# Optimization experiments

Measured on AMD Instinct MI355X. Metric: run time of the kernel, lower is better.

The kernel has to match this reference:

```python
import jax, jax.numpy as jnp
import numpy as np

N_NODES = 100000
N_EDGES = 600000
EMB_DIM = 128
NUM_LAYER = 3
NUM_GRAPHS = 64


def setup_inputs() -> dict:
    key = jax.random.key(0)
    ks = jax.random.split(key, 10)
    s = 1.0 / np.sqrt(EMB_DIM)  # keep activations stable through stacked GEMMs
    return {
        "x": jax.random.randint(ks[0], (N_NODES, 2), 0, 2),
        "edge_index_pos": jax.random.randint(ks[1], (2, N_EDGES), 0, N_NODES),
        "edge_index_inv": jax.random.randint(ks[2], (2, N_EDGES), 0, N_NODES),
        "batch": jnp.sort(jax.random.randint(ks[3], (N_NODES,), 0, NUM_GRAPHS)),
        "type_emb": jax.random.normal(ks[4], (14, EMB_DIM), jnp.float32),
        "output_emb": jax.random.normal(ks[5], (2, EMB_DIM), jnp.float32),
        "lin1_w": jax.random.normal(ks[6], (NUM_LAYER, 2, EMB_DIM, EMB_DIM), jnp.float32) * s,
        "lin1_b": jnp.zeros((NUM_LAYER, 2, EMB_DIM), jnp.float32),
        "lin2_w": jax.random.normal(ks[7], (NUM_LAYER, 2, EMB_DIM, EMB_DIM), jnp.float32) * s,
        "lin2_b": jnp.zeros((NUM_LAYER, 2, EMB_DIM), jnp.float32),
    }


def _gin_rel(h, ei, w1, b1, w2, b2):
    # GINConv (eps=0): MLP(x + sum_{j in N(i)} x_j); messages flow src(row0)->dst(row1)
    agg = jax.ops.segment_sum(h[ei[0]], ei[1], num_segments=h.shape[0])
    z = jax.nn.relu((h + agg) @ w1 + b1)
    return z @ w2 + b2


def reference(x, edge_index_pos, edge_index_inv, batch, type_emb, output_emb,
              lin1_w, lin1_b, lin2_w, lin2_b):
    # node input embedding: type + output-flag
    h = type_emb[x[:, 0]] + output_emb[x[:, 1]]
    num_layer = lin1_w.shape[0]
    for l in range(num_layer):  # small fixed layer loop
        hn = (_gin_rel(h, edge_index_pos, lin1_w[l, 0], lin1_b[l, 0], lin2_w[l, 0], lin2_b[l, 0])
              + _gin_rel(h, edge_index_inv, lin1_w[l, 1], lin1_b[l, 1], lin2_w[l, 1], lin2_b[l, 1]))
        h = hn if l == num_layer - 1 else jax.nn.relu(hn)  # JK='last', drop_ratio=0
    node_rep = h
    # MultiAggregation(['sum','mean','max','min']) pooling by graph id
    sum_g = jax.ops.segment_sum(node_rep, batch, num_segments=NUM_GRAPHS)
    cnt = jax.ops.segment_sum(jnp.ones((node_rep.shape[0],), node_rep.dtype), batch, num_segments=NUM_GRAPHS)
    mean_g = sum_g / jnp.maximum(cnt, 1.0)[:, None]
    max_g = jax.ops.segment_max(node_rep, batch, num_segments=NUM_GRAPHS)
    min_g = jax.ops.segment_min(node_rep, batch, num_segments=NUM_GRAPHS)
    h_graph = jnp.concatenate([sum_g, mean_g, max_g, min_g], axis=1)  # [B, 4*D]
    h_graph = h_graph.reshape(NUM_GRAPHS, -1, 4).transpose(0, 2, 1)   # [B, 4, D] (interleaved as in torch view)
    batch_mask = jnp.ones((NUM_GRAPHS, 4), dtype=bool)
    return (h_graph, batch_mask)
```

## Files before the change

kernel.cpp:

```cpp
#include <hip/hip_runtime.h>
#include <stdint.h>

#define M_NODES 100000
#define M_PAD   100096
#define NE      600000
#define DIM     128
#define NGRAPH  64
#define SCAN_B  512
#define SCAN_NB ((M_NODES + SCAN_B - 1) / SCAN_B)
#define WP      136

typedef __attribute__((ext_vector_type(8))) short short8;
typedef __attribute__((ext_vector_type(4))) float f32x4;
typedef __attribute__((ext_vector_type(4))) unsigned int u32x4;

__device__ inline float bf2lo(uint32_t u) { return __uint_as_float(u << 16); }
__device__ inline float bf2hi(uint32_t u) { return __uint_as_float(u & 0xffff0000u); }
__device__ inline uint32_t packbf2(float a, float b) {
    uint32_t ua = __float_as_uint(a), ub = __float_as_uint(b);
    ua += 0x7fffu + ((ua >> 16) & 1u);
    ub += 0x7fffu + ((ub >> 16) & 1u);
    return (ua >> 16) | (ub & 0xffff0000u);
}
__device__ inline uint16_t ftobf16(float f) {
    uint32_t u = __float_as_uint(f);
    u += 0x7fffu + ((u >> 16) & 1u);
    return (uint16_t)(u >> 16);
}

__device__ inline void async_copy16(const uint16_t* g, uint16_t* l) {
    __builtin_amdgcn_global_load_lds(
        (const __attribute__((address_space(1))) uint32_t*)g,
        (__attribute__((address_space(3))) uint32_t*)l, 16, 0, 0);
}

__device__ inline u32x4 gload16(const u32x4* p) {
    u32x4 r;
    asm volatile("global_load_dwordx4 %0, %1, off" : "=&v"(r) : "v"(p));
    return r;
}

#define GB_EMBED 25000
#define GB_TRANS (GB_EMBED + 12)
#define GB_ZERO  (GB_TRANS + 391)
#define GB_BOUND (GB_ZERO + 391)
__global__ void k_setup(const int* __restrict__ x, const float2* __restrict__ te2,
                        const float2* __restrict__ oe2, uint32_t* __restrict__ h2,
                        const float* __restrict__ w1, const float* __restrict__ w2,
                        uint16_t* __restrict__ wfrag,
                        const int* __restrict__ batch, int* __restrict__ starts,
                        int* __restrict__ degp, int* __restrict__ degi) {
    int b = blockIdx.x, t = threadIdx.x;
    if (b < GB_EMBED) {
        int id = b * 256 + t;
        int node = id >> 6, p = id & 63;
        int x0 = x[node * 2], x1 = x[node * 2 + 1];
        float2 a = te2[x0 * 64 + p], bb = oe2[x1 * 64 + p];
        h2[node * 64 + p] = packbf2(a.x + bb.x, a.y + bb.y);
    } else if (b < GB_TRANS) {
        int m = b - GB_EMBED;
        const float* src;
        uint16_t* dst;
        if (m < 6) {
            int L = m >> 1, rel = m & 1;
            src = w1 + m * 16384;
            dst = wfrag + (size_t)(L * 4 + rel) * 16384;
        } else {
            int mm = m - 6, L = mm >> 1, rel = mm & 1;
            src = w2 + mm * 16384;
            dst = wfrag + (size_t)(L * 4 + 2 + rel) * 16384;
        }
        for (int o = t; o < 16384; o += 256) {
            int f = o >> 3, j = o & 7;
            int fb = f >> 6, ln = f & 63;
            int t_ = fb >> 2, s_ = fb & 3, qq = ln >> 4, ll = ln & 15;
            dst[o] = ftobf16(src[(s_ * 32 + qq * 8 + j) * 128 + t_ * 16 + ll]);
        }
    } else if (b < GB_ZERO) {
        int i = (b - GB_TRANS) * 256 + t;
        if (i < M_NODES) { degp[i] = 0; degi[i] = 0; }
    } else {
        int i = (b - GB_ZERO) * 256 + t;
        if (i >= M_NODES) return;
        int bb = batch[i];
        int pb = (i == 0) ? -1 : batch[i - 1];
        for (int g = pb + 1; g <= bb; ++g) starts[g] = i;
        if (i == M_NODES - 1)
            for (int g = bb + 1; g <= NGRAPH; ++g) starts[g] = M_NODES;
    }
}

__global__ void k_hist(const int* __restrict__ ep, const int* __restrict__ ei,
                       int* __restrict__ degp, int* __restrict__ degi,
                       int* __restrict__ slotp, int* __restrict__ sloti) {
    int e = blockIdx.x * blockDim.x + threadIdx.x;
    if (e >= NE) return;
    slotp[e] = atomicAdd(&degp[ep[NE + e]], 1);
    sloti[e] = atomicAdd(&degi[ei[NE + e]], 1);
}

__global__ void k_scan1(const int* __restrict__ degp, const int* __restrict__ degi,
                        int* __restrict__ rsp, int* __restrict__ rsi, int* __restrict__ bsum) {
    __shared__ int s[SCAN_B];
    int list = blockIdx.y;
    const int* deg = list ? degi : degp;
    int* rs = list ? rsi : rsp;
    int i = blockIdx.x * SCAN_B + threadIdx.x;
    int v = (i < M_NODES) ? deg[i] : 0;
    s[threadIdx.x] = v;
    __syncthreads();
    for (int off = 1; off < SCAN_B; off <<= 1) {
        int xv = (threadIdx.x >= off) ? s[threadIdx.x - off] : 0;
        __syncthreads();
        s[threadIdx.x] += xv;
        __syncthreads();
    }
    if (i < M_NODES) rs[i + 1] = s[threadIdx.x];
    if (threadIdx.x == SCAN_B - 1) bsum[list * SCAN_NB + blockIdx.x] = s[threadIdx.x];
}

__global__ void k_scan2(const int* __restrict__ bsum, int* __restrict__ boff) {
    __shared__ int s[256];
    int list = blockIdx.x, t = threadIdx.x;
    int v = (t < SCAN_NB) ? bsum[list * SCAN_NB + t] : 0;
    s[t] = v;
    __syncthreads();
    for (int off = 1; off < 256; off <<= 1) {
        int xv = (t >= off) ? s[t - off] : 0;
        __syncthreads();
        s[t] += xv;
        __syncthreads();
    }
    if (t < SCAN_NB) boff[list * SCAN_NB + t] = s[t] - v;
}

__global__ void k_scan3(int* __restrict__ rsp, int* __restrict__ rsi, const int* __restrict__ boff) {
    int list = blockIdx.y;
    int* rs = list ? rsi : rsp;
    int i = blockIdx.x * SCAN_B + threadIdx.x;
    if (i < M_NODES) rs[i + 1] += boff[list * SCAN_NB + blockIdx.x];
    if (i == 0 && list == 0) { rsp[0] = 0; rsi[0] = 0; }
}

__global__ void k_fill(const int* __restrict__ ep, const int* __restrict__ ei,
                       const int* __restrict__ rsp, const int* __restrict__ rsi,
                       const int* __restrict__ slotp, const int* __restrict__ sloti,
                       int* __restrict__ csrp, int* __restrict__ csri) {
    int e = blockIdx.x * blockDim.x + threadIdx.x;
    if (e >= NE) return;
    int dp = ep[NE + e], sp = ep[e], kp = slotp[e];
    int di = ei[NE + e], si = ei[e], ki = sloti[e];
    csrp[rsp[dp] + kp] = sp;
    csri[rsi[di] + ki] = si;
}

__device__ inline void add8v(float* a, u32x4 v) {
    a[0] += bf2lo(v[0]); a[1] += bf2hi(v[0]);
    a[2] += bf2lo(v[1]); a[3] += bf2hi(v[1]);
    a[4] += bf2lo(v[2]); a[5] += bf2hi(v[2]);
    a[6] += bf2lo(v[3]); a[7] += bf2hi(v[3]);
}

#define AGG_W 3
__global__ void k_aggregate2(const u32x4* __restrict__ h4,
                             const int* __restrict__ rsp, const int* __restrict__ csrp,
                             const int* __restrict__ rsi, const int* __restrict__ csri,
                             u32x4* __restrict__ up, u32x4* __restrict__ ui) {
    int id = blockIdx.x * blockDim.x + threadIdx.x;
    int node = id >> 4, p = id & 15;
    if (node >= M_NODES) return;
    u32x4 hv = h4[(size_t)node * 16 + p];
    float a[8] = {bf2lo(hv[0]), bf2hi(hv[0]), bf2lo(hv[1]), bf2hi(hv[1]),
                  bf2lo(hv[2]), bf2hi(hv[2]), bf2lo(hv[3]), bf2hi(hv[3])};
    float b[8];
#pragma unroll
    for (int j = 0; j < 8; ++j) b[j] = a[j];
    int ea = rsp[node], e1a = rsp[node + 1];
    int eb = rsi[node], e1b = rsi[node + 1];
    int la = max(e1a - 1, 0);
    int lb = max(e1b - 1, 0);
    int da = e1a - ea, db = e1b - eb;
    int work = max(da, db);
    for (int done = 0; done < work; done += AGG_W) {
        int i0 = csrp[min(ea + done + 0, la)];
        int i1 = csrp[min(ea + done + 1, la)];
        int i2 = csrp[min(ea + done + 2, la)];
        int j0 = csri[min(eb + done + 0, lb)];
        int j1 = csri[min(eb + done + 1, lb)];
        int j2 = csri[min(eb + done + 2, lb)];
        u32x4 va0 = gload16(h4 + ((size_t)i0 * 16 + p));
        u32x4 va1 = gload16(h4 + ((size_t)i1 * 16 + p));
        u32x4 va2 = gload16(h4 + ((size_t)i2 * 16 + p));
        u32x4 vb0 = gload16(h4 + ((size_t)j0 * 16 + p));
        u32x4 vb1 = gload16(h4 + ((size_t)j1 * 16 + p));
        u32x4 vb2 = gload16(h4 + ((size_t)j2 * 16 + p));
        asm volatile("s_waitcnt vmcnt(0)"
                     : "+v"(va0), "+v"(va1), "+v"(va2),
                       "+v"(vb0), "+v"(vb1), "+v"(vb2));
        const u32x4 z4 = {0u, 0u, 0u, 0u};
        add8v(a, (done + 0 < da) ? va0 : z4);
        add8v(a, (done + 1 < da) ? va1 : z4);
        add8v(a, (done + 2 < da) ? va2 : z4);
        add8v(b, (done + 0 < db) ? vb0 : z4);
        add8v(b, (done + 1 < db) ? vb1 : z4);
        add8v(b, (done + 2 < db) ? vb2 : z4);
    }
    u32x4 oa, ob;
    oa[0] = packbf2(a[0], a[1]); oa[1] = packbf2(a[2], a[3]);
    oa[2] = packbf2(a[4], a[5]); oa[3] = packbf2(a[6], a[7]);
    ob[0] = packbf2(b[0], b[1]); ob[1] = packbf2(b[2], b[3]);
    ob[2] = packbf2(b[4], b[5]); ob[3] = packbf2(b[6], b[7]);
    up[(size_t)node * 16 + p] = oa;
    ui[(size_t)node * 16 + p] = ob;
}

__launch_bounds__(256, 2)
__global__ void k_gemm2(const uint16_t* __restrict__ Up, const uint16_t* __restrict__ Ui,
                        const uint16_t* __restrict__ WF1p, const float* __restrict__ B1p,
                        const uint16_t* __restrict__ WF2p, const float* __restrict__ B2p,
                        const uint16_t* __restrict__ WF1i, const float* __restrict__ B1i,
                        const uint16_t* __restrict__ WF2i, const float* __restrict__ B2i,
                        float* __restrict__ HN, uint16_t* __restrict__ HOUT, int last) {
    __shared__ __align__(16) uint16_t wbuf[16384];
    __shared__ __align__(16) uint16_t sZ[2][64 * WP];
    int tid = threadIdx.x;
    int wave = tid >> 6, lane = tid & 63;
    int q = lane >> 4, l16 = lane & 15;
    int rb0 = blockIdx.x * 128 + wave * 16;
    int rb1 = rb0 + 64;

    auto loadA = [&](const uint16_t* U, int rowbase, short8* v) {
        const uint16_t* P = U + (size_t)(rowbase + l16) * DIM + q * 8;
#pragma unroll
        for (int s = 0; s < 4; ++s) v[s] = *(const short8*)(P + s * 32);
    };
    auto loadw = [&](const uint16_t* WF) {
#pragma unroll
        for (int k = 0; k < 8; ++k)
            async_copy16(WF + (size_t)(tid + k * 256) * 8,
                         &wbuf[(size_t)wave * 512 + (size_t)k * 2048]);
    };
    auto stage1 = [&](const short8* af, const float* B1, int zslot) {
        f32x4 acc1[8];
#pragma unroll
        for (int t = 0; t < 8; ++t) acc1[t] = (f32x4){0.f, 0.f, 0.f, 0.f};
#pragma unroll
        for (int t = 0; t < 8; ++t)
#pragma unroll
            for (int s = 0; s < 4; ++s) {
                short8 bb = *(const short8*)&wbuf[((t * 4 + s) * 64 + lane) * 8];
                acc1[t] = __builtin_amdgcn_mfma_f32_16x16x32_bf16(af[s], bb, acc1[t], 0, 0, 0);
            }
#pragma unroll
        for (int t = 0; t < 8; ++t) {
            float b1v = B1[t * 16 + l16];
#pragma unroll
            for (int r = 0; r < 4; ++r)
                sZ[zslot][(wave * 16 + q * 4 + r) * WP + t * 16 + l16] =
                    ftobf16(fmaxf(acc1[t][r] + b1v, 0.f));
        }
    };
    auto stage2 = [&](int zslot, f32x4* acc2) {
        short8 zf[4];
#pragma unroll
        for (int s = 0; s < 4; ++s)
            zf[s] = *(const short8*)&sZ[zslot][(wave * 16 + l16) * WP + s * 32 + q * 8];
#pragma unroll
        for (int t = 0; t < 8; ++t)
#pragma unroll
            for (int s = 0; s < 4; ++s) {
                short8 bb = *(const short8*)&wbuf[((t * 4 + s) * 64 + lane) * 8];
                acc2[t] = __builtin_amdgcn_mfma_f32_16x16x32_bf16(zf[s], bb, acc2[t], 0, 0, 0);
            }
    };

    f32x4 acc2a[8], acc2b[8];
#pragma unroll
    for (int t = 0; t < 8; ++t) { acc2a[t] = (f32x4){0.f,0.f,0.f,0.f}; acc2b[t] = (f32x4){0.f,0.f,0.f,0.f}; }

    short8 af0[4], af1[4];
    loadw(WF1p);
    loadA(Up, rb0, af0); loadA(Up, rb1, af1);
    __syncthreads();
    stage1(af0, B1p, 0); stage1(af1, B1p, 1);
    __syncthreads();
    loadw(WF2p); __syncthreads();
    stage2(0, acc2a); stage2(1, acc2b);
    __syncthreads();
    loadw(WF1i);
    loadA(Ui, rb0, af0); loadA(Ui, rb1, af1);
    __syncthreads();
    stage1(af0, B1i, 0); stage1(af1, B1i, 1);
    __syncthreads();
    loadw(WF2i); __syncthreads();
    stage2(0, acc2a); stage2(1, acc2b);

#pragma unroll
    for (int t = 0; t < 8; ++t) {
        int col = t * 16 + l16;
        float b2v = B2p[col] + B2i[col];
#pragma unroll
        for (int r = 0; r < 4; ++r) {
            int row0 = rb0 + q * 4 + r, row1 = rb1 + q * 4 + r;
            float y0 = acc2a[t][r] + b2v, y1 = acc2b[t][r] + b2v;
            if (last) {
                HN[(size_t)row0 * DIM + col] = y0;
                HN[(size_t)row1 * DIM + col] = y1;
            } else {
                HOUT[(size_t)row0 * DIM + col] = ftobf16(fmaxf(y0, 0.f));
                HOUT[(size_t)row1 * DIM + col] = ftobf16(fmaxf(y1, 0.f));
            }
        }
    }
}

__global__ void k_pool1(const float* __restrict__ HN, const int* __restrict__ starts,
                        float* __restrict__ psum, float* __restrict__ pmax, float* __restrict__ pmin) {
    int g = blockIdx.x, sp = blockIdx.y, t = threadIdx.x;
    int d = t & 127, rh = t >> 7;
    int slot = sp * 2 + rh;
    int s0 = starts[g], s1 = starts[g + 1];
    float s = 0.f, mx = -INFINITY, mn = INFINITY;
    for (int i = s0 + slot; i < s1; i += 32) {
        float v = HN[(size_t)i * DIM + d];
        s += v; mx = fmaxf(mx, v); mn = fminf(mn, v);
    }
    int o = (g * 32 + slot) * DIM + d;
    psum[o] = s; pmax[o] = mx; pmin[o] = mn;
}

__global__ void k_pool2(const float* __restrict__ psum, const float* __restrict__ pmax,
                        const float* __restrict__ pmin, const int* __restrict__ starts,
                        float* __restrict__ out) {
    __shared__ float S[4][128];
    int g = blockIdx.x, t = threadIdx.x;
    float s = 0.f, mx = -INFINITY, mn = INFINITY;
    for (int p = 0; p < 32; ++p) {
        int o = (g * 32 + p) * DIM + t;
        s += psum[o]; mx = fmaxf(mx, pmax[o]); mn = fminf(mn, pmin[o]);
    }
    float cnt = (float)(starts[g + 1] - starts[g]);
    float mean = s / fmaxf(cnt, 1.f);
    S[0][t] = s; S[1][t] = mean; S[2][t] = mx; S[3][t] = mn;
    __syncthreads();
#pragma unroll
    for (int k = 0; k < 4; ++k) {
        int j = 4 * t + k;
        out[g * 512 + k * 128 + t] = S[j >> 7][j & 127];
    }
    if (t < 4) out[NGRAPH * 512 + g * 4 + t] = 1.0f;
}

extern "C" void kernel_launch(void* const* d_in, const int* in_sizes, int n_in,
                              void* d_out, int out_size, void* d_ws, size_t ws_size,
                              hipStream_t stream) {
    const int* x     = (const int*)d_in[0];
    const int* ep    = (const int*)d_in[1];
    const int* ei    = (const int*)d_in[2];
    const int* batch = (const int*)d_in[3];
    const float* te  = (const float*)d_in[4];
    const float* oe  = (const float*)d_in[5];
    const float* w1  = (const float*)d_in[6];
    const float* b1  = (const float*)d_in[7];
    const float* w2  = (const float*)d_in[8];
    const float* b2  = (const float*)d_in[9];
    float* out = (float*)d_out;

    char* w = (char*)d_ws;
    auto alloc = [&](size_t n) { char* p = w; w += (n + 255) & ~(size_t)255; return p; };
    uint16_t* h_bf  = (uint16_t*)alloc((size_t)M_PAD * DIM * 2);
    uint16_t* u_pos = (uint16_t*)alloc((size_t)M_PAD * DIM * 2);
    uint16_t* u_inv = (uint16_t*)alloc((size_t)M_PAD * DIM * 2);
    float*    hn    = (float*)alloc((size_t)M_PAD * DIM * 4);
    uint16_t* wfrag = (uint16_t*)alloc((size_t)12 * 16384 * 2);
    int* rsp  = (int*)alloc((M_NODES + 2) * 4);
    int* rsi  = (int*)alloc((M_NODES + 2) * 4);
    int* degp = (int*)alloc(M_NODES * 4);
    int* degi = (int*)alloc(M_NODES * 4);
    int* csrp = (int*)alloc((size_t)NE * 4);
    int* csri = (int*)alloc((size_t)NE * 4);
    int* bsum = (int*)alloc(2 * SCAN_NB * 4);
    int* boff = (int*)alloc(2 * SCAN_NB * 4);
    int* starts = (int*)alloc((NGRAPH + 1) * 4);
    float* psum = (float*)alloc(NGRAPH * 32 * DIM * 4);
    float* pmax = (float*)alloc(NGRAPH * 32 * DIM * 4);
    float* pmin = (float*)alloc(NGRAPH * 32 * DIM * 4);
    if ((size_t)(w - (char*)d_ws) > ws_size) return;

    int* slotp = (int*)u_pos;
    int* sloti = (int*)u_inv;

    k_setup<<<GB_BOUND, 256, 0, stream>>>(x, (const float2*)te, (const float2*)oe,
                                          (uint32_t*)h_bf, w1, w2, wfrag,
                                          batch, starts, degp, degi);
    k_hist<<<(NE + 255) / 256, 256, 0, stream>>>(ep, ei, degp, degi, slotp, sloti);
    dim3 gs(SCAN_NB, 2);
    k_scan1<<<gs, SCAN_B, 0, stream>>>(degp, degi, rsp, rsi, bsum);
    k_scan2<<<2, 256, 0, stream>>>(bsum, boff);
    k_scan3<<<gs, SCAN_B, 0, stream>>>(rsp, rsi, boff);
    k_fill<<<(NE + 255) / 256, 256, 0, stream>>>(ep, ei, rsp, rsi, slotp, sloti, csrp, csri);

    for (int l = 0; l < 3; ++l) {
        k_aggregate2<<<(M_NODES * 16 + 255) / 256, 256, 0, stream>>>(
            (const u32x4*)h_bf, rsp, csrp, rsi, csri, (u32x4*)u_pos, (u32x4*)u_inv);
        const uint16_t* wfL = wfrag + (size_t)l * 4 * 16384;
        k_gemm2<<<M_PAD / 128, 256, 0, stream>>>(
            u_pos, u_inv,
            wfL,              b1 + (2 * l) * 128,
            wfL + 2 * 16384,  b2 + (2 * l) * 128,
            wfL + 16384,      b1 + (2 * l + 1) * 128,
            wfL + 3 * 16384,  b2 + (2 * l + 1) * 128,
            hn, h_bf, (l == 2) ? 1 : 0);
    }
    dim3 gp(NGRAPH, 16);
    k_pool1<<<gp, 256, 0, stream>>>(hn, starts, psum, pmax, pmin);
    k_pool2<<<NGRAPH, 128, 0, stream>>>(psum, pmax, pmin, starts, out);
}
```

Baseline: 456.5 us.

## Bucket-sort nodes by degree to balance aggregation work across wavefronts

Adds a counting sort of nodes keyed on the larger of their two in-degrees, producing a permutation that the aggregation kernel uses to pick which node each group of 16 lanes handles. Nodes with similar degree then share a wavefront, which is meant to cut divergence in the neighbor loop. The cost is three extra small kernels with atomics, plus an indirect lookup per node that scatters the h reads and the output writes. Atomic slot order within a bucket is nondeterministic, but the results are not affected.

```diff
diff --git a/kernel.cpp b/kernel.cpp
--- a/kernel.cpp
+++ b/kernel.cpp
@@ -9,6 +9,7 @@
 #define SCAN_B  512
 #define SCAN_NB ((M_NODES + SCAN_B - 1) / SCAN_B)
 #define WP      136
+#define DBUCKET 64
 
 typedef __attribute__((ext_vector_type(8))) short short8;
 typedef __attribute__((ext_vector_type(4))) float f32x4;
@@ -49,7 +50,8 @@
                         const float* __restrict__ w1, const float* __restrict__ w2,
                         uint16_t* __restrict__ wfrag,
                         const int* __restrict__ batch, int* __restrict__ starts,
-                        int* __restrict__ degp, int* __restrict__ degi) {
+                        int* __restrict__ degp, int* __restrict__ degi,
+                        int* __restrict__ dcnt, int* __restrict__ dcur) {
     int b = blockIdx.x, t = threadIdx.x;
     if (b < GB_EMBED) {
         int id = b * 256 + t;
@@ -79,6 +81,7 @@
     } else if (b < GB_ZERO) {
         int i = (b - GB_TRANS) * 256 + t;
         if (i < M_NODES) { degp[i] = 0; degi[i] = 0; }
+        if (b == GB_TRANS && t < DBUCKET) { dcnt[t] = 0; dcur[t] = 0; }
     } else {
         int i = (b - GB_ZERO) * 256 + t;
         if (i >= M_NODES) return;
@@ -140,6 +143,39 @@
     int i = blockIdx.x * SCAN_B + threadIdx.x;
     if (i < M_NODES) rs[i + 1] += boff[list * SCAN_NB + blockIdx.x];
     if (i == 0 && list == 0) { rsp[0] = 0; rsi[0] = 0; }
+}
+
+__global__ void k_dsort1(const int* __restrict__ degp, const int* __restrict__ degi,
+                         int* __restrict__ dcnt) {
+    int i = blockIdx.x * blockDim.x + threadIdx.x;
+    if (i >= M_NODES) return;
+    int key = min(max(degp[i], degi[i]), DBUCKET - 1);
+    atomicAdd(&dcnt[key], 1);
+}
+
+__global__ void k_dsort2(const int* __restrict__ dcnt, int* __restrict__ dbase) {
+    __shared__ int s[DBUCKET];
+    int t = threadIdx.x;
+    int v = dcnt[t];
+    s[t] = v;
+    __syncthreads();
+    for (int off = 1; off < DBUCKET; off <<= 1) {
+        int xv = (t >= off) ? s[t - off] : 0;
+        __syncthreads();
+        s[t] += xv;
+        __syncthreads();
+    }
+    dbase[t] = s[t] - v;
+}
+
+__global__ void k_dsort3(const int* __restrict__ degp, const int* __restrict__ degi,
+                         const int* __restrict__ dbase, int* __restrict__ dcur,
+                         int* __restrict__ ord) {
+    int i = blockIdx.x * blockDim.x + threadIdx.x;
+    if (i >= M_NODES) return;
+    int key = min(max(degp[i], degi[i]), DBUCKET - 1);
+    int pos = atomicAdd(&dcur[key], 1);
+    ord[dbase[key] + pos] = i;
 }
 
 __global__ void k_fill(const int* __restrict__ ep, const int* __restrict__ ei,
@@ -162,13 +198,14 @@
 }
 
 #define AGG_W 3
-__global__ void k_aggregate2(const u32x4* __restrict__ h4,
+__global__ void k_aggregate2(const u32x4* __restrict__ h4, const int* __restrict__ ord,
                              const int* __restrict__ rsp, const int* __restrict__ csrp,
                              const int* __restrict__ rsi, const int* __restrict__ csri,
                              u32x4* __restrict__ up, u32x4* __restrict__ ui) {
     int id = blockIdx.x * blockDim.x + threadIdx.x;
-    int node = id >> 4, p = id & 15;
-    if (node >= M_NODES) return;
+    int slot = id >> 4, p = id & 15;
+    if (slot >= M_NODES) return;
+    int node = ord[slot];
     u32x4 hv = h4[(size_t)node * 16 + p];
     float a[8] = {bf2lo(hv[0]), bf2hi(hv[0]), bf2lo(hv[1]), bf2hi(hv[1]),
                   bf2lo(hv[2]), bf2hi(hv[2]), bf2lo(hv[3]), bf2hi(hv[3])};
@@ -385,6 +422,10 @@
     float* psum = (float*)alloc(NGRAPH * 32 * DIM * 4);
     float* pmax = (float*)alloc(NGRAPH * 32 * DIM * 4);
     float* pmin = (float*)alloc(NGRAPH * 32 * DIM * 4);
+    int* ord   = (int*)alloc(M_NODES * 4);
+    int* dcnt  = (int*)alloc(DBUCKET * 4);
+    int* dbase = (int*)alloc(DBUCKET * 4);
+    int* dcur  = (int*)alloc(DBUCKET * 4);
     if ((size_t)(w - (char*)d_ws) > ws_size) return;
 
     int* slotp = (int*)u_pos;
@@ -392,17 +433,20 @@
 
     k_setup<<<GB_BOUND, 256, 0, stream>>>(x, (const float2*)te, (const float2*)oe,
                                           (uint32_t*)h_bf, w1, w2, wfrag,
-                                          batch, starts, degp, degi);
+                                          batch, starts, degp, degi, dcnt, dcur);
     k_hist<<<(NE + 255) / 256, 256, 0, stream>>>(ep, ei, degp, degi, slotp, sloti);
     dim3 gs(SCAN_NB, 2);
     k_scan1<<<gs, SCAN_B, 0, stream>>>(degp, degi, rsp, rsi, bsum);
     k_scan2<<<2, 256, 0, stream>>>(bsum, boff);
     k_scan3<<<gs, SCAN_B, 0, stream>>>(rsp, rsi, boff);
+    k_dsort1<<<(M_NODES + 255) / 256, 256, 0, stream>>>(degp, degi, dcnt);
+    k_dsort2<<<1, DBUCKET, 0, stream>>>(dcnt, dbase);
+    k_dsort3<<<(M_NODES + 255) / 256, 256, 0, stream>>>(degp, degi, dbase, dcur, ord);
     k_fill<<<(NE + 255) / 256, 256, 0, stream>>>(ep, ei, rsp, rsi, slotp, sloti, csrp, csri);
 
     for (int l = 0; l < 3; ++l) {
         k_aggregate2<<<(M_NODES * 16 + 255) / 256, 256, 0, stream>>>(
-            (const u32x4*)h_bf, rsp, csrp, rsi, csri, (u32x4*)u_pos, (u32x4*)u_inv);
+            (const u32x4*)h_bf, ord, rsp, csrp, rsi, csri, (u32x4*)u_pos, (u32x4*)u_inv);
         const uint16_t* wfL = wfrag + (size_t)l * 4 * 16384;
         k_gemm2<<<M_PAD / 128, 256, 0, stream>>>(
             u_pos, u_inv,
```

Result: slower. 1.254 ms (+174.8%).

## Sort nodes by degree bucket to balance aggregation wavefront work

Applied to the files above, without the earlier changes.

Adds a three-kernel counting sort that orders node ids by max(pos,inv) in-degree, capped at 64 buckets. The aggregation kernel then processes nodes in this order, so wavefronts hold nodes with similar degree and lose fewer lanes to divergence. The cost is three extra small launches, including a serial single-block scan, plus one indirection load per node. Output writes and h reads become scattered instead of contiguous, which may hurt coalescing.

```diff
diff --git a/kernel.cpp b/kernel.cpp
--- a/kernel.cpp
+++ b/kernel.cpp
@@ -9,6 +9,8 @@
 #define SCAN_B  512
 #define SCAN_NB ((M_NODES + SCAN_B - 1) / SCAN_B)
 #define WP      136
+#define DBUCKET 64
+#define DSORT_NBLK ((M_NODES + 255) / 256)
 
 typedef __attribute__((ext_vector_type(8))) short short8;
 typedef __attribute__((ext_vector_type(4))) float f32x4;
@@ -142,6 +144,60 @@
     if (i == 0 && list == 0) { rsp[0] = 0; rsi[0] = 0; }
 }
 
+__global__ void k_dsort1(const int* __restrict__ degp, const int* __restrict__ degi,
+                         int* __restrict__ bh) {
+    __shared__ int hist[DBUCKET];
+    int t = threadIdx.x, blk = blockIdx.x;
+    if (t < DBUCKET) hist[t] = 0;
+    __syncthreads();
+    int i = blk * 256 + t;
+    if (i < M_NODES) {
+        int key = min(max(degp[i], degi[i]), DBUCKET - 1);
+        atomicAdd(&hist[key], 1);
+    }
+    __syncthreads();
+    if (t < DBUCKET) bh[t * DSORT_NBLK + blk] = hist[t];
+}
+
+__global__ void k_dsort2(const int* __restrict__ bh, int* __restrict__ bbase) {
+    __shared__ int s[256];
+    __shared__ int carry;
+    int t = threadIdx.x;
+    if (t == 0) carry = 0;
+    __syncthreads();
+    const int N = DBUCKET * DSORT_NBLK;
+    for (int base = 0; base < N; base += 256) {
+        int i = base + t;
+        int v = (i < N) ? bh[i] : 0;
+        s[t] = v;
+        __syncthreads();
+        for (int off = 1; off < 256; off <<= 1) {
+            int xv = (t >= off) ? s[t - off] : 0;
+            __syncthreads();
+            s[t] += xv;
+            __syncthreads();
+        }
+        if (i < N) bbase[i] = carry + s[t] - v;
+        __syncthreads();
+        if (t == 255) carry += s[255];
+        __syncthreads();
+    }
+}
+
+__global__ void k_dsort3(const int* __restrict__ degp, const int* __restrict__ degi,
+                         const int* __restrict__ bbase, int* __restrict__ ord) {
+    __shared__ int hist[DBUCKET];
+    int t = threadIdx.x, blk = blockIdx.x;
+    if (t < DBUCKET) hist[t] = 0;
+    __syncthreads();
+    int i = blk * 256 + t;
+    if (i < M_NODES) {
+        int key = min(max(degp[i], degi[i]), DBUCKET - 1);
+        int rank = atomicAdd(&hist[key], 1);
+        ord[bbase[key * DSORT_NBLK + blk] + rank] = i;
+    }
+}
+
 __global__ void k_fill(const int* __restrict__ ep, const int* __restrict__ ei,
                        const int* __restrict__ rsp, const int* __restrict__ rsi,
                        const int* __restrict__ slotp, const int* __restrict__ sloti,
@@ -162,13 +218,14 @@
 }
 
 #define AGG_W 3
-__global__ void k_aggregate2(const u32x4* __restrict__ h4,
+__global__ void k_aggregate2(const u32x4* __restrict__ h4, const int* __restrict__ ord,
                              const int* __restrict__ rsp, const int* __restrict__ csrp,
                              const int* __restrict__ rsi, const int* __restrict__ csri,
                              u32x4* __restrict__ up, u32x4* __restrict__ ui) {
     int id = blockIdx.x * blockDim.x + threadIdx.x;
-    int node = id >> 4, p = id & 15;
-    if (node >= M_NODES) return;
+    int slot = id >> 4, p = id & 15;
+    if (slot >= M_NODES) return;
+    int node = ord[slot];
     u32x4 hv = h4[(size_t)node * 16 + p];
     float a[8] = {bf2lo(hv[0]), bf2hi(hv[0]), bf2lo(hv[1]), bf2hi(hv[1]),
                   bf2lo(hv[2]), bf2hi(hv[2]), bf2lo(hv[3]), bf2hi(hv[3])};
@@ -385,6 +442,9 @@
     float* psum = (float*)alloc(NGRAPH * 32 * DIM * 4);
     float* pmax = (float*)alloc(NGRAPH * 32 * DIM * 4);
     float* pmin = (float*)alloc(NGRAPH * 32 * DIM * 4);
+    int* ord   = (int*)alloc(M_NODES * 4);
+    int* bh    = (int*)alloc(DBUCKET * DSORT_NBLK * 4);
+    int* bbase = (int*)alloc(DBUCKET * DSORT_NBLK * 4);
     if ((size_t)(w - (char*)d_ws) > ws_size) return;
 
     int* slotp = (int*)u_pos;
@@ -398,11 +458,14 @@
     k_scan1<<<gs, SCAN_B, 0, stream>>>(degp, degi, rsp, rsi, bsum);
     k_scan2<<<2, 256, 0, stream>>>(bsum, boff);
     k_scan3<<<gs, SCAN_B, 0, stream>>>(rsp, rsi, boff);
+    k_dsort1<<<DSORT_NBLK, 256, 0, stream>>>(degp, degi, bh);
+    k_dsort2<<<1, 256, 0, stream>>>(bh, bbase);
+    k_dsort3<<<DSORT_NBLK, 256, 0, stream>>>(degp, degi, bbase, ord);
     k_fill<<<(NE + 255) / 256, 256, 0, stream>>>(ep, ei, rsp, rsi, slotp, sloti, csrp, csri);
 
     for (int l = 0; l < 3; ++l) {
         k_aggregate2<<<(M_NODES * 16 + 255) / 256, 256, 0, stream>>>(
-            (const u32x4*)h_bf, rsp, csrp, rsi, csri, (u32x4*)u_pos, (u32x4*)u_inv);
+            (const u32x4*)h_bf, ord, rsp, csrp, rsi, csri, (u32x4*)u_pos, (u32x4*)u_inv);
         const uint16_t* wfL = wfrag + (size_t)l * 4 * 16384;
         k_gemm2<<<M_PAD / 128, 256, 0, stream>>>(
             u_pos, u_inv,
```

Result: slower. 584.3 us (+28.0%).

## Fuse neighbor aggregation into the GIN MLP GEMM kernel via LDS staging

Applied to the files above, without the earlier changes.

The separate aggregation kernel is folded into the GEMM kernel. Each 128-row block now gathers neighbor sums for its own rows, writes the bf16 results to shared memory and feeds them straight into the MFMA stages. This removes the global write and re-read of the two aggregated buffers and one launch per layer, and h is ping-ponged between two buffers to avoid a read-after-write hazard. In exchange the GEMM blocks carry the irregular gather latency, have fewer threads available to hide it, and use more LDS, which may lower occupancy.

```diff
diff --git a/kernel.cpp b/kernel.cpp
--- a/kernel.cpp
+++ b/kernel.cpp
@@ -161,79 +161,87 @@
     a[6] += bf2lo(v[3]); a[7] += bf2hi(v[3]);
 }
 
-#define AGG_W 3
-__global__ void k_aggregate2(const u32x4* __restrict__ h4,
-                             const int* __restrict__ rsp, const int* __restrict__ csrp,
-                             const int* __restrict__ rsi, const int* __restrict__ csri,
-                             u32x4* __restrict__ up, u32x4* __restrict__ ui) {
-    int id = blockIdx.x * blockDim.x + threadIdx.x;
-    int node = id >> 4, p = id & 15;
-    if (node >= M_NODES) return;
-    u32x4 hv = h4[(size_t)node * 16 + p];
-    float a[8] = {bf2lo(hv[0]), bf2hi(hv[0]), bf2lo(hv[1]), bf2hi(hv[1]),
-                  bf2lo(hv[2]), bf2hi(hv[2]), bf2lo(hv[3]), bf2hi(hv[3])};
-    float b[8];
-#pragma unroll
-    for (int j = 0; j < 8; ++j) b[j] = a[j];
-    int ea = rsp[node], e1a = rsp[node + 1];
-    int eb = rsi[node], e1b = rsi[node + 1];
-    int la = max(e1a - 1, 0);
-    int lb = max(e1b - 1, 0);
-    int da = e1a - ea, db = e1b - eb;
-    int work = max(da, db);
-    for (int done = 0; done < work; done += AGG_W) {
-        int i0 = csrp[min(ea + done + 0, la)];
-        int i1 = csrp[min(ea + done + 1, la)];
-        int i2 = csrp[min(ea + done + 2, la)];
-        int j0 = csri[min(eb + done + 0, lb)];
-        int j1 = csri[min(eb + done + 1, lb)];
-        int j2 = csri[min(eb + done + 2, lb)];
-        u32x4 va0 = gload16(h4 + ((size_t)i0 * 16 + p));
-        u32x4 va1 = gload16(h4 + ((size_t)i1 * 16 + p));
-        u32x4 va2 = gload16(h4 + ((size_t)i2 * 16 + p));
-        u32x4 vb0 = gload16(h4 + ((size_t)j0 * 16 + p));
-        u32x4 vb1 = gload16(h4 + ((size_t)j1 * 16 + p));
-        u32x4 vb2 = gload16(h4 + ((size_t)j2 * 16 + p));
-        asm volatile("s_waitcnt vmcnt(0)"
-                     : "+v"(va0), "+v"(va1), "+v"(va2),
-                       "+v"(vb0), "+v"(vb1), "+v"(vb2));
-        const u32x4 z4 = {0u, 0u, 0u, 0u};
-        add8v(a, (done + 0 < da) ? va0 : z4);
-        add8v(a, (done + 1 < da) ? va1 : z4);
-        add8v(a, (done + 2 < da) ? va2 : z4);
-        add8v(b, (done + 0 < db) ? vb0 : z4);
-        add8v(b, (done + 1 < db) ? vb1 : z4);
-        add8v(b, (done + 2 < db) ? vb2 : z4);
-    }
-    u32x4 oa, ob;
-    oa[0] = packbf2(a[0], a[1]); oa[1] = packbf2(a[2], a[3]);
-    oa[2] = packbf2(a[4], a[5]); oa[3] = packbf2(a[6], a[7]);
-    ob[0] = packbf2(b[0], b[1]); ob[1] = packbf2(b[2], b[3]);
-    ob[2] = packbf2(b[4], b[5]); ob[3] = packbf2(b[6], b[7]);
-    up[(size_t)node * 16 + p] = oa;
-    ui[(size_t)node * 16 + p] = ob;
-}
-
 __launch_bounds__(256, 2)
-__global__ void k_gemm2(const uint16_t* __restrict__ Up, const uint16_t* __restrict__ Ui,
-                        const uint16_t* __restrict__ WF1p, const float* __restrict__ B1p,
-                        const uint16_t* __restrict__ WF2p, const float* __restrict__ B2p,
-                        const uint16_t* __restrict__ WF1i, const float* __restrict__ B1i,
-                        const uint16_t* __restrict__ WF2i, const float* __restrict__ B2i,
-                        float* __restrict__ HN, uint16_t* __restrict__ HOUT, int last) {
-    __shared__ __align__(16) uint16_t wbuf[16384];
-    __shared__ __align__(16) uint16_t sZ[2][64 * WP];
+__global__ void k_gemmagg(const u32x4* __restrict__ h4,
+                          const int* __restrict__ rsp, const int* __restrict__ csrp,
+                          const int* __restrict__ rsi, const int* __restrict__ csri,
+                          const uint16_t* __restrict__ WF1p, const float* __restrict__ B1p,
+                          const uint16_t* __restrict__ WF2p, const float* __restrict__ B2p,
+                          const uint16_t* __restrict__ WF1i, const float* __restrict__ B1i,
+                          const uint16_t* __restrict__ WF2i, const float* __restrict__ B2i,
+                          float* __restrict__ HN, uint16_t* __restrict__ HOUT, int last) {
+    __shared__ __align__(16) char smem[67584];
+    uint16_t* uLDS = (uint16_t*)smem;
+    uint16_t* wbuf = (uint16_t*)smem;
+    uint16_t* sZ   = (uint16_t*)(smem + 32768);
+
     int tid = threadIdx.x;
     int wave = tid >> 6, lane = tid & 63;
     int q = lane >> 4, l16 = lane & 15;
-    int rb0 = blockIdx.x * 128 + wave * 16;
-    int rb1 = rb0 + 64;
-
-    auto loadA = [&](const uint16_t* U, int rowbase, short8* v) {
-        const uint16_t* P = U + (size_t)(rowbase + l16) * DIM + q * 8;
-#pragma unroll
-        for (int s = 0; s < 4; ++s) v[s] = *(const short8*)(P + s * 32);
-    };
+    int rbase = blockIdx.x * 128;
+
+    for (int k = 0; k < 8; ++k) {
+        int task = k * 256 + tid;
+        int row = task >> 4, p = task & 15;
+        int nd = rbase + row;
+        int node = min(nd, M_NODES - 1);
+        u32x4 hv = h4[(size_t)node * 16 + p];
+        int ea = rsp[node], e1a = rsp[node + 1];
+        int eb = rsi[node], e1b = rsi[node + 1];
+        int la = max(e1a - 1, 0), lb = max(e1b - 1, 0);
+        int da = e1a - ea, db = e1b - eb;
+        if (nd >= M_NODES) { da = 0; db = 0; hv = (u32x4){0u, 0u, 0u, 0u}; }
+        float a[8] = {bf2lo(hv[0]), bf2hi(hv[0]), bf2lo(hv[1]), bf2hi(hv[1]),
+                      bf2lo(hv[2]), bf2hi(hv[2]), bf2lo(hv[3]), bf2hi(hv[3])};
+        float b[8];
+#pragma unroll
+        for (int j = 0; j < 8; ++j) b[j] = a[j];
+        int work = max(da, db);
+        for (int done = 0; done < work; done += 3) {
+            int i0 = csrp[min(ea + done + 0, la)];
+            int i1 = csrp[min(ea + done + 1, la)];
+            int i2 = csrp[min(ea + done + 2, la)];
+            int j0 = csri[min(eb + done + 0, lb)];
+            int j1 = csri[min(eb + done + 1, lb)];
+            int j2 = csri[min(eb + done + 2, lb)];
+            u32x4 va0 = gload16(h4 + ((size_t)i0 * 16 + p));
+            u32x4 va1 = gload16(h4 + ((size_t)i1 * 16 + p));
+            u32x4 va2 = gload16(h4 + ((size_t)i2 * 16 + p));
+            u32x4 vb0 = gload16(h4 + ((size_t)j0 * 16 + p));
+            u32x4 vb1 = gload16(h4 + ((size_t)j1 * 16 + p));
+            u32x4 vb2 = gload16(h4 + ((size_t)j2 * 16 + p));
+            asm volatile("s_waitcnt vmcnt(0)"
+                         : "+v"(va0), "+v"(va1), "+v"(va2),
+                           "+v"(vb0), "+v"(vb1), "+v"(vb2));
+            const u32x4 z4 = {0u, 0u, 0u, 0u};
+            add8v(a, (done + 0 < da) ? va0 : z4);
+            add8v(a, (done + 1 < da) ? va1 : z4);
+            add8v(a, (done + 2 < da) ? va2 : z4);
+            add8v(b, (done + 0 < db) ? vb0 : z4);
+            add8v(b, (done + 1 < db) ? vb1 : z4);
+            add8v(b, (done + 2 < db) ? vb2 : z4);
+        }
+        u32x4 oa, ob;
+        oa[0] = packbf2(a[0], a[1]); oa[1] = packbf2(a[2], a[3]);
+        oa[2] = packbf2(a[4], a[5]); oa[3] = packbf2(a[6], a[7]);
+        ob[0] = packbf2(b[0], b[1]); ob[1] = packbf2(b[2], b[3]);
+        ob[2] = packbf2(b[4], b[5]); ob[3] = packbf2(b[6], b[7]);
+        *(u32x4*)&uLDS[(size_t)row * 128 + p * 8] = oa;
+        *(u32x4*)&uLDS[16384 + (size_t)row * 128 + p * 8] = ob;
+    }
+    __syncthreads();
+
+    short8 afp0[4], afp1[4], afi0[4], afi1[4];
+    int r0 = wave * 16 + l16, r1 = r0 + 64;
+#pragma unroll
+    for (int s = 0; s < 4; ++s) {
+        afp0[s] = *(const short8*)&uLDS[(size_t)r0 * 128 + s * 32 + q * 8];
+        afp1[s] = *(const short8*)&uLDS[(size_t)r1 * 128 + s * 32 + q * 8];
+        afi0[s] = *(const short8*)&uLDS[16384 + (size_t)r0 * 128 + s * 32 + q * 8];
+        afi1[s] = *(const short8*)&uLDS[16384 + (size_t)r1 * 128 + s * 32 + q * 8];
+    }
+    __syncthreads();
+
     auto loadw = [&](const uint16_t* WF) {
 #pragma unroll
         for (int k = 0; k < 8; ++k)
@@ -256,7 +264,7 @@
             float b1v = B1[t * 16 + l16];
 #pragma unroll
             for (int r = 0; r < 4; ++r)
-                sZ[zslot][(wave * 16 + q * 4 + r) * WP + t * 16 + l16] =
+                sZ[zslot * 8704 + (wave * 16 + q * 4 + r) * WP + t * 16 + l16] =
                     ftobf16(fmaxf(acc1[t][r] + b1v, 0.f));
         }
     };
@@ -264,7 +272,7 @@
         short8 zf[4];
 #pragma unroll
         for (int s = 0; s < 4; ++s)
-            zf[s] = *(const short8*)&sZ[zslot][(wave * 16 + l16) * WP + s * 32 + q * 8];
+            zf[s] = *(const short8*)&sZ[zslot * 8704 + (wave * 16 + l16) * WP + s * 32 + q * 8];
 #pragma unroll
         for (int t = 0; t < 8; ++t)
 #pragma unroll
@@ -278,23 +286,19 @@
 #pragma unroll
     for (int t = 0; t < 8; ++t) { acc2a[t] = (f32x4){0.f,0.f,0.f,0.f}; acc2b[t] = (f32x4){0.f,0.f,0.f,0.f}; }
 
-    short8 af0[4], af1[4];
-    loadw(WF1p);
-    loadA(Up, rb0, af0); loadA(Up, rb1, af1);
-    __syncthreads();
-    stage1(af0, B1p, 0); stage1(af1, B1p, 1);
+    loadw(WF1p); __syncthreads();
+    stage1(afp0, B1p, 0); stage1(afp1, B1p, 1);
     __syncthreads();
     loadw(WF2p); __syncthreads();
     stage2(0, acc2a); stage2(1, acc2b);
     __syncthreads();
-    loadw(WF1i);
-    loadA(Ui, rb0, af0); loadA(Ui, rb1, af1);
-    __syncthreads();
-    stage1(af0, B1i, 0); stage1(af1, B1i, 1);
+    loadw(WF1i); __syncthreads();
+    stage1(afi0, B1i, 0); stage1(afi1, B1i, 1);
     __syncthreads();
     loadw(WF2i); __syncthreads();
     stage2(0, acc2a); stage2(1, acc2b);
 
+    int rb0 = rbase + wave * 16, rb1 = rb0 + 64;
 #pragma unroll
     for (int t = 0; t < 8; ++t) {
         int col = t * 16 + l16;
@@ -368,9 +372,8 @@
 
     char* w = (char*)d_ws;
     auto alloc = [&](size_t n) { char* p = w; w += (n + 255) & ~(size_t)255; return p; };
-    uint16_t* h_bf  = (uint16_t*)alloc((size_t)M_PAD * DIM * 2);
-    uint16_t* u_pos = (uint16_t*)alloc((size_t)M_PAD * DIM * 2);
-    uint16_t* u_inv = (uint16_t*)alloc((size_t)M_PAD * DIM * 2);
+    uint16_t* h_b0  = (uint16_t*)alloc((size_t)M_PAD * DIM * 2);
+    uint16_t* h_b1  = (uint16_t*)alloc((size_t)M_PAD * DIM * 2);
     float*    hn    = (float*)alloc((size_t)M_PAD * DIM * 4);
     uint16_t* wfrag = (uint16_t*)alloc((size_t)12 * 16384 * 2);
     int* rsp  = (int*)alloc((M_NODES + 2) * 4);
@@ -387,11 +390,11 @@
     float* pmin = (float*)alloc(NGRAPH * 32 * DIM * 4);
     if ((size_t)(w - (char*)d_ws) > ws_size) return;
 
-    int* slotp = (int*)u_pos;
-    int* sloti = (int*)u_inv;
+    int* slotp = (int*)hn;
+    int* sloti = (int*)hn + NE;
 
     k_setup<<<GB_BOUND, 256, 0, stream>>>(x, (const float2*)te, (const float2*)oe,
-                                          (uint32_t*)h_bf, w1, w2, wfrag,
+                                          (uint32_t*)h_b0, w1, w2, wfrag,
                                           batch, starts, degp, degi);
     k_hist<<<(NE + 255) / 256, 256, 0, stream>>>(ep, ei, degp, degi, slotp, sloti);
     dim3 gs(SCAN_NB, 2);
@@ -401,16 +404,16 @@
     k_fill<<<(NE + 255) / 256, 256, 0, stream>>>(ep, ei, rsp, rsi, slotp, sloti, csrp, csri);
 
     for (int l = 0; l < 3; ++l) {
-        k_aggregate2<<<(M_NODES * 16 + 255) / 256, 256, 0, stream>>>(
-            (const u32x4*)h_bf, rsp, csrp, rsi, csri, (u32x4*)u_pos, (u32x4*)u_inv);
         const uint16_t* wfL = wfrag + (size_t)l * 4 * 16384;
-        k_gemm2<<<M_PAD / 128, 256, 0, stream>>>(
-            u_pos, u_inv,
+        const uint16_t* hin = (l & 1) ? h_b1 : h_b0;
+        uint16_t* hout = (l & 1) ? h_b0 : h_b1;
+        k_gemmagg<<<M_PAD / 128, 256, 0, stream>>>(
+            (const u32x4*)hin, rsp, csrp, rsi, csri,
             wfL,              b1 + (2 * l) * 128,
             wfL + 2 * 16384,  b2 + (2 * l) * 128,
             wfL + 16384,      b1 + (2 * l + 1) * 128,
             wfL + 3 * 16384,  b2 + (2 * l + 1) * 128,
-            hn, h_bf, (l == 2) ? 1 : 0);
+            hn, hout, (l == 2) ? 1 : 0);
     }
     dim3 gp(NGRAPH, 16);
     k_pool1<<<gp, 256, 0, stream>>>(hn, starts, psum, pmax, pmin);
```

New measurement: 491.2 us. 1.08x slower.
